# Performance work log

Measured on AMD Instinct MI355X. Metric: run time of the kernel, lower is better.

The kernel has to match this reference:

```python
import jax, jax.numpy as jnp
import numpy as np

D_MODEL = 512
NUM_HEADS = 8
D_K = D_MODEL // NUM_HEADS
B, N = 8192, 14

_SENSOR_DIST = np.array([
 [0,1,4,1,1,2,1,2,1,3,2,1,3,5],[1,0,3,1,2,1,2,1,2,2,3,2,2,4],
 [4,3,0,3,5,4,3,2,5,5,6,5,1,1],[1,1,3,0,2,2,1,1,2,3,3,2,2,4],
 [1,2,5,2,0,3,2,3,1,4,1,2,4,6],[2,1,4,2,3,0,3,2,3,1,4,3,3,5],
 [1,2,3,1,2,3,0,1,2,4,3,2,2,4],[2,1,2,1,3,2,1,0,3,3,4,3,1,3],
 [1,2,5,2,1,3,2,3,0,4,2,2,4,6],[3,2,5,3,4,1,4,3,4,0,5,4,4,6],
 [2,3,6,3,1,4,3,4,2,5,0,3,5,7],[1,2,5,2,2,3,2,3,2,4,3,0,4,6],
 [3,2,1,2,4,3,2,1,4,4,5,4,0,2],[5,4,1,4,6,5,4,3,6,6,7,6,2,0]], dtype=np.float32)


def setup_inputs() -> dict:
    key = jax.random.key(0)
    ks = jax.random.split(key, 10)
    s = 1.0 / np.sqrt(D_MODEL)
    inp = {
        "x": jax.random.normal(ks[0], (B, N, D_MODEL), dtype=jnp.float32),
        "Wq": jax.random.uniform(ks[1], (D_MODEL, D_MODEL), minval=-s, maxval=s),
        "bq": jax.random.uniform(ks[2], (D_MODEL,), minval=-s, maxval=s),
        "Wk": jax.random.uniform(ks[3], (D_MODEL, D_MODEL), minval=-s, maxval=s),
        "bk": jax.random.uniform(ks[4], (D_MODEL,), minval=-s, maxval=s),
        "Wv": jax.random.uniform(ks[5], (D_MODEL, D_MODEL), minval=-s, maxval=s),
        "bv": jax.random.uniform(ks[6], (D_MODEL,), minval=-s, maxval=s),
        "Wo": jax.random.uniform(ks[7], (D_MODEL, D_MODEL), minval=-s, maxval=s),
        "bo": jax.random.uniform(ks[8], (D_MODEL,), minval=-s, maxval=s),
        "scale": jnp.array(1.0, dtype=jnp.float32),
        "power": jnp.array(1.0, dtype=jnp.float32),
        "dist": jnp.asarray(_SENSOR_DIST),
    }
    return inp


def _safe_pow(d, p):
    # d ** p with d >= 0; guard log(0) on the zero diagonal (forward identical)
    pos = d > 0
    return jnp.where(pos, jnp.exp(p * jnp.log(jnp.where(pos, d, 1.0))), 0.0)


def reference(x, Wq, bq, Wk, bk, Wv, bv, Wo, bo, scale, power, dist):
    b, n, _ = x.shape
    def split(h):  # [B,N,D] -> [B,H,N,dk]
        return h.reshape(b, n, NUM_HEADS, D_K).transpose(0, 2, 1, 3)
    Q = split(x @ Wq.T + bq)
    K = split(x @ Wk.T + bk)
    V = split(x @ Wv.T + bv)
    scores = jnp.einsum("bhnd,bhmd->bhnm", Q, K) / jnp.sqrt(jnp.float32(D_K))
    prior = scale / (1.0 + _safe_pow(dist[:n, :n], power))  # [N,N]
    attn = jax.nn.softmax(scores * prior[None, None], axis=-1)
    out = jnp.einsum("bhnm,bhmd->bhnd", attn, V)
    out = out.transpose(0, 2, 1, 3).reshape(b, n, D_MODEL)
    return out @ Wo.T + bo
```

## Files before the change

kernel.cpp:

```cpp
#include <hip/hip_runtime.h>
#include <stdint.h>

#define D_MODEL 512
#define NHEADS 8
#define DK 64
#define NB 8192
#define NTOK 14
#define ROWS (NB*NTOK)

typedef unsigned short ushort_t;
typedef __attribute__((ext_vector_type(8))) short short8;
typedef __attribute__((ext_vector_type(4))) short short4v;
typedef __attribute__((ext_vector_type(4))) float f32x4;

__device__ __forceinline__ float bf2f(ushort_t u) {
    return __uint_as_float(((unsigned int)u) << 16);
}
__device__ __forceinline__ ushort_t f2bf(float f) {
    unsigned int u = __float_as_uint(f);
    unsigned int r = (u + 0x7FFFu + ((u >> 16) & 1u)) >> 16;
    return (ushort_t)r;
}

__global__ void cvt_kernel(const float* __restrict__ src, ushort_t* __restrict__ dst, int n)
{
    int i = (blockIdx.x * blockDim.x + threadIdx.x) * 4;
    if (i + 3 < n) {
        float4 v = *(const float4*)(src + i);
        short4v o;
        o[0] = (short)f2bf(v.x);
        o[1] = (short)f2bf(v.y);
        o[2] = (short)f2bf(v.z);
        o[3] = (short)f2bf(v.w);
        *(short4v*)(dst + i) = o;
    }
}

__global__ __launch_bounds__(256, 2) void gemm_bt(
    const ushort_t* __restrict__ A, int lda,
    const ushort_t* __restrict__ W0, const ushort_t* __restrict__ W1, const ushort_t* __restrict__ W2,
    const float* __restrict__ b0, const float* __restrict__ b1, const float* __restrict__ b2,
    ushort_t* __restrict__ Cb, float* __restrict__ Cf, int ldc)
{
    __shared__ __align__(16) ushort_t As[128 * 32];
    __shared__ __align__(16) ushort_t Bs[128 * 32];

    const int m0 = blockIdx.x * 128;
    const int n0 = blockIdx.y * 128;
    const int wsel = n0 >> 9;
    const ushort_t* W    = (wsel == 0) ? W0 : ((wsel == 1) ? W1 : W2);
    const float*    bias = (wsel == 0) ? b0 : ((wsel == 1) ? b1 : b2);
    const int nw = n0 & 511;

    const int tid  = threadIdx.x;
    const int lane = tid & 63;
    const int wave = tid >> 6;
    const int quad = lane >> 4;
    const int c    = lane & 15;
    const int wm   = (wave & 1) * 64;
    const int wn   = (wave >> 1) * 64;

    f32x4 acc[4][4];
    #pragma unroll
    for (int i = 0; i < 4; ++i)
        #pragma unroll
        for (int j = 0; j < 4; ++j)
            acc[i][j] = (f32x4){0.f, 0.f, 0.f, 0.f};

    for (int k0 = 0; k0 < 512; k0 += 32) {
        #pragma unroll
        for (int r = 0; r < 2; ++r) {
            int cidx = r * 256 + tid;
            int row  = cidx >> 2;
            int kq   = (cidx & 3) * 8;
            *(short8*)&As[row * 32 + kq] =
                *(const short8*)(A + (size_t)(m0 + row) * lda + k0 + kq);
            *(short8*)&Bs[row * 32 + kq] =
                *(const short8*)(W + (size_t)(nw + row) * 512 + k0 + kq);
        }
        __syncthreads();

        short8 af[4], bfr[4];
        #pragma unroll
        for (int i = 0; i < 4; ++i) {
            af[i]  = *(const short8*)&As[(wm + i * 16 + c) * 32 + quad * 8];
            bfr[i] = *(const short8*)&Bs[(wn + i * 16 + c) * 32 + quad * 8];
        }
        #pragma unroll
        for (int i = 0; i < 4; ++i)
            #pragma unroll
            for (int j = 0; j < 4; ++j)
                acc[i][j] = __builtin_amdgcn_mfma_f32_16x16x32_bf16(af[i], bfr[j], acc[i][j], 0, 0, 0);
        __syncthreads();
    }

    #pragma unroll
    for (int j = 0; j < 4; ++j) {
        int coln = wn + j * 16 + c;
        float bv = bias[nw + coln];
        int col  = n0 + coln;
        #pragma unroll
        for (int i = 0; i < 4; ++i) {
            #pragma unroll
            for (int r = 0; r < 4; ++r) {
                int row = m0 + wm + i * 16 + quad * 4 + r;
                float v = acc[i][j][r] + bv;
                if (Cf) Cf[(size_t)row * ldc + col] = v;
                else    Cb[(size_t)row * ldc + col] = f2bf(v);
            }
        }
    }
}

__global__ __launch_bounds__(256, 4) void attn_kernel(
    const ushort_t* __restrict__ QKV,
    const float* __restrict__ dist,
    const float* __restrict__ scale_p,
    const float* __restrict__ power_p,
    ushort_t* __restrict__ O)
{
    __shared__ __align__(16) ushort_t Pl[4][16 * 32];

    const int tid  = threadIdx.x;
    const int lane = tid & 63;
    const int wave = tid >> 6;
    const int id   = blockIdx.x * 4 + wave;
    const int b    = id >> 3;
    const int h    = id & 7;
    const int quad = lane >> 4;
    const int c    = lane & 15;

    const float scale = scale_p[0];
    const float power = power_p[0];

    const size_t rowbase = (size_t)b * NTOK;
    const int mrow = (c < NTOK) ? c : (NTOK - 1);

    const ushort_t* qp = QKV + (rowbase + mrow) * 1536 + h * 64 + quad * 8;
    short8 aq0 = *(const short8*)qp;
    short8 aq1 = *(const short8*)(qp + 32);
    const ushort_t* kp = QKV + (rowbase + mrow) * 1536 + 512 + h * 64 + quad * 8;
    short8 bk0 = *(const short8*)kp;
    short8 bk1 = *(const short8*)(kp + 32);

    f32x4 S = (f32x4){0.f, 0.f, 0.f, 0.f};
    S = __builtin_amdgcn_mfma_f32_16x16x32_bf16(aq0, bk0, S, 0, 0, 0);
    S = __builtin_amdgcn_mfma_f32_16x16x32_bf16(aq1, bk1, S, 0, 0, 0);

    float p4[4];
    #pragma unroll
    for (int r = 0; r < 4; ++r) {
        int row = quad * 4 + r;
        float s;
        if (c < NTOK && row < NTOK) {
            float d  = dist[row * NTOK + c];
            float dp = (d > 0.f) ? __expf(power * __logf(d)) : 0.f;
            float pri = scale / (1.f + dp);
            s = S[r] * 0.125f * pri;
        } else if (row >= NTOK) {
            s = 0.f;
        } else {
            s = -INFINITY;
        }
        float smax = s;
        #pragma unroll
        for (int off = 1; off < 16; off <<= 1)
            smax = fmaxf(smax, __shfl_xor(smax, off));
        float e = (c < NTOK) ? __expf(s - smax) : 0.f;
        float l = e;
        #pragma unroll
        for (int off = 1; off < 16; off <<= 1)
            l += __shfl_xor(l, off);
        p4[r] = e / l;
    }

    #pragma unroll
    for (int z = 0; z < 4; ++z) {
        int idx = lane * 4 + z;
        int zr = idx >> 4, zc = idx & 15;
        Pl[wave][zr * 32 + 16 + zc] = 0;
    }
    #pragma unroll
    for (int r = 0; r < 4; ++r)
        Pl[wave][(quad * 4 + r) * 32 + c] = f2bf(p4[r]);
    __syncthreads();

    short8 pf = *(const short8*)&Pl[wave][c * 32 + quad * 8];

    const ushort_t* Vb = QKV + rowbase * 1536 + 1024 + h * 64;
    f32x4 o[4];
    #pragma unroll
    for (int t = 0; t < 4; ++t) {
        short8 vf = (short8){0, 0, 0, 0, 0, 0, 0, 0};
        #pragma unroll
        for (int j = 0; j < 8; ++j) {
            int m = quad * 8 + j;
            if (m < NTOK)
                vf[j] = (short)Vb[(size_t)m * 1536 + t * 16 + c];
        }
        f32x4 z = (f32x4){0.f, 0.f, 0.f, 0.f};
        o[t] = __builtin_amdgcn_mfma_f32_16x16x32_bf16(pf, vf, z, 0, 0, 0);
    }

    #pragma unroll
    for (int r = 0; r < 4; ++r) {
        int row = quad * 4 + r;
        if (row < NTOK) {
            #pragma unroll
            for (int t = 0; t < 4; ++t)
                O[(rowbase + row) * 512 + h * 64 + t * 16 + c] = f2bf(o[t][r]);
        }
    }
}

extern "C" void kernel_launch(void* const* d_in, const int* in_sizes, int n_in,
                              void* d_out, int out_size, void* d_ws, size_t ws_size,
                              hipStream_t stream)
{
    const float* x     = (const float*)d_in[0];
    const float* Wq    = (const float*)d_in[1];
    const float* bq    = (const float*)d_in[2];
    const float* Wk    = (const float*)d_in[3];
    const float* bk    = (const float*)d_in[4];
    const float* Wv    = (const float*)d_in[5];
    const float* bv    = (const float*)d_in[6];
    const float* Wo    = (const float*)d_in[7];
    const float* bo    = (const float*)d_in[8];
    const float* scale = (const float*)d_in[9];
    const float* power = (const float*)d_in[10];
    const float* dist  = (const float*)d_in[11];

    float* out = (float*)d_out;

    ushort_t* xb  = (ushort_t*)d_ws;
    ushort_t* wb  = xb + (size_t)ROWS * 512;
    ushort_t* qkv = wb + (size_t)4 * 512 * 512;

    dim3 blk(256);

    const int NX = ROWS * 512;
    const int NW = 512 * 512;
    cvt_kernel<<<NX / 1024, blk, 0, stream>>>(x,  xb, NX);
    cvt_kernel<<<NW / 1024, blk, 0, stream>>>(Wq, wb + 0 * (size_t)NW, NW);
    cvt_kernel<<<NW / 1024, blk, 0, stream>>>(Wk, wb + 1 * (size_t)NW, NW);
    cvt_kernel<<<NW / 1024, blk, 0, stream>>>(Wv, wb + 2 * (size_t)NW, NW);
    cvt_kernel<<<NW / 1024, blk, 0, stream>>>(Wo, wb + 3 * (size_t)NW, NW);

    dim3 g1(ROWS / 128, 1536 / 128);
    gemm_bt<<<g1, blk, 0, stream>>>(xb, 512,
                                    wb, wb + (size_t)NW, wb + 2 * (size_t)NW,
                                    bq, bk, bv, qkv, nullptr, 1536);

    dim3 g2((NB * NHEADS) / 4);
    attn_kernel<<<g2, blk, 0, stream>>>(qkv, dist, scale, power, xb);

    dim3 g3(ROWS / 128, 512 / 128);
    gemm_bt<<<g3, blk, 0, stream>>>(xb, 512,
                                    wb + 3 * (size_t)NW, wb + 3 * (size_t)NW, wb + 3 * (size_t)NW,
                                    bo, bo, bo, nullptr, out, 512);
}
```

Measured before the change: 1.042 ms.

## Use direct global-to-LDS loads, LDS-staged coalesced epilogue, and swapped grid order

The GEMM tile loads now use global_load_lds, so data goes from global memory straight into shared memory without passing through registers. The epilogue first stages the accumulators plus bias in a padded LDS buffer, then writes rows back as 16-byte vectors instead of scattered 2- or 4-byte stores. The grid axes are swapped so blocks that share the same A rows run next to each other, which should improve L2 reuse of A. The cost is extra LDS (about 36KB more per block), which may lower occupancy, and the async-LDS layout has to match the fragment read pattern.

After: 952.4 us. -8.6%, faster.

```diff
diff --git a/kernel.cpp b/kernel.cpp
--- a/kernel.cpp
+++ b/kernel.cpp
@@ -20,6 +20,13 @@
     unsigned int u = __float_as_uint(f);
     unsigned int r = (u + 0x7FFFu + ((u >> 16) & 1u)) >> 16;
     return (ushort_t)r;
+}
+
+__device__ __forceinline__ void async_copy16(const ushort_t* g, ushort_t* l) {
+    __builtin_amdgcn_global_load_lds(
+        (const __attribute__((address_space(1))) void*)g,
+        (__attribute__((address_space(3))) void*)l,
+        16, 0, 0);
 }
 
 __global__ void cvt_kernel(const float* __restrict__ src, ushort_t* __restrict__ dst, int n)
@@ -44,9 +51,10 @@
 {
     __shared__ __align__(16) ushort_t As[128 * 32];
     __shared__ __align__(16) ushort_t Bs[128 * 32];
-
-    const int m0 = blockIdx.x * 128;
-    const int n0 = blockIdx.y * 128;
+    __shared__ __align__(16) char Ep[4 * 32 * 72 * 4];
+
+    const int m0 = blockIdx.y * 128;
+    const int n0 = blockIdx.x * 128;
     const int wsel = n0 >> 9;
     const ushort_t* W    = (wsel == 0) ? W0 : ((wsel == 1) ? W1 : W2);
     const float*    bias = (wsel == 0) ? b0 : ((wsel == 1) ? b1 : b2);
@@ -69,14 +77,13 @@
 
     for (int k0 = 0; k0 < 512; k0 += 32) {
         #pragma unroll
-        for (int r = 0; r < 2; ++r) {
-            int cidx = r * 256 + tid;
-            int row  = cidx >> 2;
-            int kq   = (cidx & 3) * 8;
-            *(short8*)&As[row * 32 + kq] =
-                *(const short8*)(A + (size_t)(m0 + row) * lda + k0 + kq);
-            *(short8*)&Bs[row * 32 + kq] =
-                *(const short8*)(W + (size_t)(nw + row) * 512 + k0 + kq);
+        for (int rnd = 0; rnd < 2; ++rnd) {
+            int chunk = rnd * 256 + wave * 64 + lane;
+            int row   = chunk >> 2;
+            int kq    = (chunk & 3) * 8;
+            int lbase = (rnd * 256 + wave * 64) * 8;
+            async_copy16(A + (size_t)(m0 + row) * lda + k0 + kq, &As[lbase]);
+            async_copy16(W + (size_t)(nw + row) * 512 + k0 + kq, &Bs[lbase]);
         }
         __syncthreads();
 
@@ -94,19 +101,46 @@
         __syncthreads();
     }
 
-    #pragma unroll
-    for (int j = 0; j < 4; ++j) {
-        int coln = wn + j * 16 + c;
-        float bv = bias[nw + coln];
-        int col  = n0 + coln;
-        #pragma unroll
-        for (int i = 0; i < 4; ++i) {
-            #pragma unroll
-            for (int r = 0; r < 4; ++r) {
-                int row = m0 + wm + i * 16 + quad * 4 + r;
-                float v = acc[i][j][r] + bv;
-                if (Cf) Cf[(size_t)row * ldc + col] = v;
-                else    Cb[(size_t)row * ldc + col] = f2bf(v);
+    if (Cf == nullptr) {
+        ushort_t* sl = (ushort_t*)Ep + wave * 64 * 72;
+        #pragma unroll
+        for (int i = 0; i < 4; ++i)
+            #pragma unroll
+            for (int j = 0; j < 4; ++j)
+                #pragma unroll
+                for (int r = 0; r < 4; ++r) {
+                    int rl = i * 16 + quad * 4 + r;
+                    int cl = j * 16 + c;
+                    sl[rl * 72 + cl] = f2bf(acc[i][j][r] + bias[nw + wn + cl]);
+                }
+        #pragma unroll
+        for (int t = 0; t < 8; ++t) {
+            int rl = t * 8 + (lane >> 3);
+            int cl = (lane & 7) * 8;
+            short8 v = *(const short8*)&sl[rl * 72 + cl];
+            *(short8*)&Cb[(size_t)(m0 + wm + rl) * ldc + n0 + wn + cl] = v;
+        }
+    } else {
+        float* slf = (float*)Ep + wave * 32 * 72;
+        #pragma unroll
+        for (int half = 0; half < 2; ++half) {
+            #pragma unroll
+            for (int i2 = 0; i2 < 2; ++i2)
+                #pragma unroll
+                for (int j = 0; j < 4; ++j)
+                    #pragma unroll
+                    for (int r = 0; r < 4; ++r) {
+                        int i  = half * 2 + i2;
+                        int rl = i2 * 16 + quad * 4 + r;
+                        int cl = j * 16 + c;
+                        slf[rl * 72 + cl] = acc[i][j][r] + bias[nw + wn + cl];
+                    }
+            #pragma unroll
+            for (int t = 0; t < 8; ++t) {
+                int rl = t * 4 + (lane >> 4);
+                int cl = (lane & 15) * 4;
+                f32x4 v = *(const f32x4*)&slf[rl * 72 + cl];
+                *(f32x4*)&Cf[(size_t)(m0 + wm + half * 32 + rl) * ldc + n0 + wn + cl] = v;
             }
         }
     }
@@ -246,7 +280,7 @@
     cvt_kernel<<<NW / 1024, blk, 0, stream>>>(Wv, wb + 2 * (size_t)NW, NW);
     cvt_kernel<<<NW / 1024, blk, 0, stream>>>(Wo, wb + 3 * (size_t)NW, NW);
 
-    dim3 g1(ROWS / 128, 1536 / 128);
+    dim3 g1(1536 / 128, ROWS / 128);
     gemm_bt<<<g1, blk, 0, stream>>>(xb, 512,
                                     wb, wb + (size_t)NW, wb + 2 * (size_t)NW,
                                     bq, bk, bv, qkv, nullptr, 1536);
@@ -254,7 +288,7 @@
     dim3 g2((NB * NHEADS) / 4);
     attn_kernel<<<g2, blk, 0, stream>>>(qkv, dist, scale, power, xb);
 
-    dim3 g3(ROWS / 128, 512 / 128);
+    dim3 g3(512 / 128, ROWS / 128);
     gemm_bt<<<g3, blk, 0, stream>>>(xb, 512,
                                     wb + 3 * (size_t)NW, wb + 3 * (size_t)NW, wb + 3 * (size_t)NW,
                                     bo, bo, bo, nullptr, out, 512);
```
